# Kernel tuning notes

Measured on AMD Instinct MI355X. Metric: run time of the kernel, lower is better.

The kernel has to match this reference:

```python
import jax, jax.numpy as jnp
import numpy as np

N, M = 100000, 800000
F_IN, F_E, H = 64, 16, 64
T_NODE, T_EDGE = 2, 3
HEAD_DIM = 16.0


def setup_inputs() -> dict:
    key = jax.random.key(0)
    ks = jax.random.split(key, 16)
    inp = {
        "x": jax.random.normal(ks[0], (N, F_IN), jnp.float32),
        "edge_feat": jax.random.normal(ks[1], (M, F_E), jnp.float32),
        "node_type": jax.random.randint(ks[2], (N,), 0, T_NODE, jnp.int32),
        "edge_src": jax.random.randint(ks[3], (M,), 0, N, jnp.int32),
        "edge_dst": jax.random.randint(ks[4], (M,), 0, N, jnp.int32),
        "edge_type": jax.random.randint(ks[5], (M,), 0, T_EDGE, jnp.int32),
    }
    s_n = 1.0 / np.sqrt(F_IN)
    s_e = 1.0 / np.sqrt(F_E)
    for i, name in enumerate(["W1", "W2", "W3", "W4"]):
        inp[name] = jax.random.normal(ks[6 + i], (T_NODE, F_IN, H), jnp.float32) * s_n
        inp["b" + name[1]] = jax.random.normal(ks[10 + i], (T_NODE, H), jnp.float32) * 0.01
    inp["W5"] = jax.random.normal(ks[14], (T_EDGE, F_E, H), jnp.float32) * s_e
    inp["b5"] = jax.random.normal(ks[15], (T_EDGE, H), jnp.float32) * 0.01
    return inp


def _node_proj(x, W, b, node_type):
    # per-node-type linear: [T,F,H] weights, select row per node type
    p = jnp.einsum('nf,tfh->tnh', x, W) + b[:, None, :]      # [T,N,H]
    return jnp.take_along_axis(p, node_type[None, :, None], axis=0)[0]  # [N,H]


def reference(x, edge_feat, W1, b1, W2, b2, W3, b3, W4, b4, W5, b5,
              node_type, edge_src, edge_dst, edge_type):
    n = x.shape[0]
    h1 = _node_proj(x, W1, b1, node_type)
    h2 = _node_proj(x, W2, b2, node_type)
    h3 = _node_proj(x, W3, b3, node_type)
    h4 = _node_proj(x, W4, b4, node_type)
    # per-edge-type linear via weight gather (F_E is small)
    w5e = jnp.einsum('mf,mfh->mh', edge_feat, W5[edge_type]) + b5[edge_type]  # [M,H]
    # scalar attention logit per edge (w3_i . (w4_j + w5_ij)) / sqrt(head_dim)
    num = jnp.sum(h3[edge_dst] * (h4[edge_src] + w5e), axis=-1)  # [M]
    # softmax over a single scalar per edge == 1.0 exactly (faithful to source)
    score = jax.nn.softmax((num / jnp.sqrt(HEAD_DIM))[:, None], axis=-1)[:, 0]  # [M]
    msg = score[:, None] * (h2[edge_src] + w5e)                  # [M,H]
    out = h1 + jax.ops.segment_sum(msg, edge_dst, num_segments=n)
    return out
```

## Files before the change

kernel.cpp:

```cpp
#include <hip/hip_runtime.h>


#define CAP 16
#define OVF_CAP 32768

typedef __attribute__((ext_vector_type(8))) short short8;
typedef __attribute__((ext_vector_type(4))) float f32x4;

__device__ __forceinline__ float b2f(unsigned short u) {
    union { unsigned v; float f; } x; x.v = ((unsigned)u) << 16; return x.f;
}
__device__ __forceinline__ unsigned short f2b(float f) {
    union { float f; unsigned v; } x; x.f = f;
    unsigned u = x.v;
    unsigned r = (u + 0x7FFFu + ((u >> 16) & 1u)) >> 16;
    return (unsigned short)r;
}

__global__ __launch_bounds__(256) void k1_gemm_scatter(
    const float* __restrict__ x, const int* __restrict__ nt,
    const float* __restrict__ W1, const float* __restrict__ b1,
    const float* __restrict__ W2, const float* __restrict__ b2,
    const int* __restrict__ esrc, const int* __restrict__ edst,
    const int* __restrict__ etype,
    int* __restrict__ cnt32, int* __restrict__ ovfCnt,
    int4* __restrict__ ovf, int2* __restrict__ rec,
    float* __restrict__ out, unsigned short* __restrict__ h2b,
    int N, int M)
{
    __shared__ __align__(16) unsigned short sx[128 * 72];
    __shared__ __align__(16) unsigned short sw[4][64 * 72];
    __shared__ int snt[128];

    int tid = threadIdx.x;

    if (blockIdx.x & 1) {
        int e0 = (blockIdx.x >> 1) * 1024 + tid;
        int dd[4], ssrc[4], tty[4];
        bool v[4];
#pragma unroll
        for (int j = 0; j < 4; ++j) {
            int e = e0 + j * 256;
            v[j] = e < M;
            int ec = v[j] ? e : 0;
            dd[j]   = edst[ec];
            ssrc[j] = esrc[ec];
            tty[j]  = etype[ec];
        }
        int pos[4];
#pragma unroll
        for (int j = 0; j < 4; ++j)
            if (v[j]) pos[j] = atomicAdd(&cnt32[dd[j]], 1);
#pragma unroll
        for (int j = 0; j < 4; ++j) {
            if (!v[j]) continue;
            int packed = ssrc[j] | (tty[j] << 20);
            int e = e0 + j * 256;
            if (pos[j] < CAP) {
                rec[dd[j] * CAP + pos[j]] = make_int2(packed, e);
            } else {
                int slot = atomicAdd(ovfCnt, 1);
                if (slot < OVF_CAP) ovf[slot] = make_int4(packed, e, dd[j], 0);
            }
        }
        return;
    }

    int rowbase = (blockIdx.x >> 1) * 128;

    const float* Wm0 = W1;
    const float* Wm1 = W1 + 4096;
    const float* Wm2 = W2;
    const float* Wm3 = W2 + 4096;
#pragma unroll
    for (int j = 0; j < 4; ++j) {
        int k  = (tid >> 4) + j * 16;
        int n4 = (tid & 15) * 4;
        float4 w0 = *(const float4*)&Wm0[k * 64 + n4];
        float4 w1v = *(const float4*)&Wm1[k * 64 + n4];
        float4 w2v = *(const float4*)&Wm2[k * 64 + n4];
        float4 w3 = *(const float4*)&Wm3[k * 64 + n4];
        sw[0][(n4 + 0) * 72 + k] = f2b(w0.x);
        sw[0][(n4 + 1) * 72 + k] = f2b(w0.y);
        sw[0][(n4 + 2) * 72 + k] = f2b(w0.z);
        sw[0][(n4 + 3) * 72 + k] = f2b(w0.w);
        sw[1][(n4 + 0) * 72 + k] = f2b(w1v.x);
        sw[1][(n4 + 1) * 72 + k] = f2b(w1v.y);
        sw[1][(n4 + 2) * 72 + k] = f2b(w1v.z);
        sw[1][(n4 + 3) * 72 + k] = f2b(w1v.w);
        sw[2][(n4 + 0) * 72 + k] = f2b(w2v.x);
        sw[2][(n4 + 1) * 72 + k] = f2b(w2v.y);
        sw[2][(n4 + 2) * 72 + k] = f2b(w2v.z);
        sw[2][(n4 + 3) * 72 + k] = f2b(w2v.w);
        sw[3][(n4 + 0) * 72 + k] = f2b(w3.x);
        sw[3][(n4 + 1) * 72 + k] = f2b(w3.y);
        sw[3][(n4 + 2) * 72 + k] = f2b(w3.z);
        sw[3][(n4 + 3) * 72 + k] = f2b(w3.w);
    }

    if (tid < 128) {
        int r = rowbase + tid;
        snt[tid] = (r < N) ? nt[r] : 0;
    }

    int fr = (tid & 15) * 4;
    int ir = tid >> 4;
#pragma unroll
    for (int it = 0; it < 8; ++it) {
        int i = it * 16 + ir;
        int r = rowbase + i;
        float4 v = make_float4(0.f, 0.f, 0.f, 0.f);
        if (r < N) v = *(const float4*)&x[(size_t)r * 64 + fr];
        ushort4 p;
        p.x = f2b(v.x); p.y = f2b(v.y); p.z = f2b(v.z); p.w = f2b(v.w);
        *(ushort4*)&sx[i * 72 + fr] = p;
    }
    __syncthreads();

    int lane = tid & 63;
    int wid  = tid >> 6;
    int q    = lane >> 4;
    int cc   = lane & 15;
    int m0   = wid * 32;

    f32x4 acc[4][2][4];
#pragma unroll
    for (int mm = 0; mm < 4; ++mm)
#pragma unroll
        for (int s = 0; s < 2; ++s)
#pragma unroll
            for (int t = 0; t < 4; ++t)
                acc[mm][s][t] = (f32x4){0.f, 0.f, 0.f, 0.f};

#pragma unroll
    for (int k0 = 0; k0 < 64; k0 += 32) {
        int ko = k0 + q * 8;
        short8 af0 = *(short8*)&sx[(m0 + cc) * 72 + ko];
        short8 af1 = *(short8*)&sx[(m0 + 16 + cc) * 72 + ko];
#pragma unroll
        for (int mm = 0; mm < 4; ++mm)
#pragma unroll
            for (int t = 0; t < 4; ++t) {
                short8 bf = *(short8*)&sw[mm][(t * 16 + cc) * 72 + ko];
                acc[mm][0][t] = __builtin_amdgcn_mfma_f32_16x16x32_bf16(
                    af0, bf, acc[mm][0][t], 0, 0, 0);
                acc[mm][1][t] = __builtin_amdgcn_mfma_f32_16x16x32_bf16(
                    af1, bf, acc[mm][1][t], 0, 0, 0);
            }
    }

    float b1v[2][4], b2v[2][4];
#pragma unroll
    for (int ty = 0; ty < 2; ++ty)
#pragma unroll
        for (int t = 0; t < 4; ++t) {
            b1v[ty][t] = b1[ty * 64 + t * 16 + cc];
            b2v[ty][t] = b2[ty * 64 + t * 16 + cc];
        }

#pragma unroll
    for (int s = 0; s < 2; ++s)
#pragma unroll
        for (int reg = 0; reg < 4; ++reg) {
            int rl_ = m0 + s * 16 + q * 4 + reg;
            int r = rowbase + rl_;
            if (r < N) {
                int ty = snt[rl_];
#pragma unroll
                for (int t = 0; t < 4; ++t) {
                    float v1 = (ty ? acc[1][s][t][reg] : acc[0][s][t][reg])
                               + b1v[ty][t];
                    float v2 = (ty ? acc[3][s][t][reg] : acc[2][s][t][reg])
                               + b2v[ty][t];
                    out[(size_t)r * 64 + t * 16 + cc] = v1;
                    h2b[(size_t)r * 64 + t * 16 + cc] = f2b(v2);
                }
            }
        }
}

__global__ __launch_bounds__(256) void k2_gather_mm(
    const float* __restrict__ ef, const int2* __restrict__ rec,
    const int* __restrict__ cnt32,
    const float* __restrict__ W5, const float* __restrict__ b5,
    const int4* __restrict__ ovf, const int* __restrict__ ovfCnt,
    const unsigned short* __restrict__ h2b, float* __restrict__ out,
    int N, int gatherBlocks, int ovfBlocks)
{
    __shared__ __align__(16) unsigned short sa[32 * 136];
    __shared__ __align__(16) unsigned short swt[64 * 136];
    __shared__ __align__(16) float sH[32 * 66];

    int tid = threadIdx.x;
    int lane = tid & 63;
    int wid = tid >> 6;

    if (blockIdx.x >= (unsigned)gatherBlocks) {
        int novf = min(*ovfCnt, OVF_CAP);
        int gw = (blockIdx.x - gatherBlocks) * 4 + wid;
        int nw = ovfBlocks * 4;
        for (int ri = gw; ri < novf; ri += nw) {
            int4 o = ovf[ri];
            int s = o.x & 0xFFFFF;
            int t = (unsigned)o.x >> 20;
            float acc = b5[t * 64 + lane] + b2f(h2b[((size_t)s << 6) | lane]);
#pragma unroll
            for (int f = 0; f < 16; ++f)
                acc = fmaf(ef[(size_t)o.y * 16 + f],
                           W5[(t * 16 + f) * 64 + lane], acc);
            unsafeAtomicAdd(&out[(size_t)o.z * 64 + lane], acc);
        }
        return;
    }

#pragma unroll
    for (int k = 0; k < 13; ++k) {
        int idx = tid + k * 256;
        int j = idx >> 6;
        int h = idx & 63;
        float wv = 0.f;
        if (j < 48)      wv = W5[j * 64 + h];
        else if (j < 51) wv = b5[(j - 48) * 64 + h];
        unsigned short wb = f2b(wv);
        swt[h * 136 + j] = wb;
        swt[h * 136 + 52 + j] = wb;
    }
    {
        ushort4 z; z.x = 0; z.y = 0; z.z = 0; z.w = 0;
#pragma unroll
        for (int k = 0; k < 2; ++k) {
            int idx = tid + k * 256;
            if (idx < 384) {
                int h = idx / 6;
                int sp = (idx - h * 6) * 4;
                *(ushort4*)&swt[h * 136 + 104 + sp] = z;
            }
        }
        if (tid < 192) {
            int row = tid / 6;
            int sp = (tid - row * 6) * 4;
            *(ushort4*)&sa[row * 136 + 104 + sp] = z;
        }
    }

    int myt = (lane < 48) ? (lane >> 4) : (lane - 48);
    unsigned myf = lane & 15;
    bool fl = lane < 48;
    int wbase = blockIdx.x * 32 + wid * 8;

#pragma unroll 1
    for (int g = 0; g < 8; ++g) {
        int d = wbase + g;
        int dg = (d < N) ? min(cnt32[d], CAP) : 0;
        unsigned base = (unsigned)d * CAP;

        float accH = 0.f, accS = 0.f;
        float hLast = 0.f, vLast = 0.f;
        int tLast = -1;
        int dgm1 = dg - 1;

        for (int i = 0; i < dg; i += 8) {
            int2 r[8];
#pragma unroll
            for (int j = 0; j < 8; ++j) {
                int ij = min(i + j, dgm1);
                r[j] = rec[base + ij];
            }
            float hv[8], ev[8];
#pragma unroll
            for (int j = 0; j < 8; ++j) {
                unsigned s = (unsigned)r[j].x & 0xFFFFFu;
                hv[j] = b2f(h2b[((size_t)s << 6) | (unsigned)lane]);
                ev[j] = ef[((unsigned)r[j].y << 4) | myf];
            }
#pragma unroll
            for (int j = 0; j < 8; ++j) {
                int t = (int)((unsigned)r[j].x >> 20);
                float v = fl ? ev[j] : 1.0f;
                accH += hv[j];
                accS += (t == myt) ? v : 0.f;
                hLast = hv[j]; vLast = v; tLast = t;
            }
        }
        float fd = (float)(((dg + 7) & ~7) - dg);
        accH -= fd * hLast;
        accS -= (tLast == myt) ? fd * vLast : 0.f;

        int wd = wid * 8 + g;
        if (lane < 52) {
            unsigned short hi = f2b(accS);
            unsigned short lo = f2b(accS - b2f(hi));
            sa[wd * 136 + lane] = hi;
            sa[wd * 136 + 52 + lane] = lo;
        }
        sH[wd * 66 + lane] = accH;
    }
    __syncthreads();

    int q  = lane >> 4;
    int cc = lane & 15;
    int s  = wid & 1;
    int t0 = wid >> 1;

    f32x4 acc0 = (f32x4){0.f, 0.f, 0.f, 0.f};
    f32x4 acc1 = (f32x4){0.f, 0.f, 0.f, 0.f};
#pragma unroll
    for (int k0 = 0; k0 < 128; k0 += 32) {
        int ko = k0 + q * 8;
        short8 af = *(short8*)&sa[(s * 16 + cc) * 136 + ko];
        short8 bf0 = *(short8*)&swt[(t0 * 16 + cc) * 136 + ko];
        short8 bf1 = *(short8*)&swt[((t0 + 2) * 16 + cc) * 136 + ko];
        acc0 = __builtin_amdgcn_mfma_f32_16x16x32_bf16(af, bf0, acc0, 0, 0, 0);
        acc1 = __builtin_amdgcn_mfma_f32_16x16x32_bf16(af, bf1, acc1, 0, 0, 0);
    }

#pragma unroll
    for (int reg = 0; reg < 4; ++reg) {
        int rl = s * 16 + q * 4 + reg;
        int d = blockIdx.x * 32 + rl;
        if (d < N) {
            int c0 = t0 * 16 + cc;
            int c1 = (t0 + 2) * 16 + cc;
            float v0 = acc0[reg] + sH[rl * 66 + c0];
            float v1 = acc1[reg] + sH[rl * 66 + c1];
            unsafeAtomicAdd(&out[(size_t)d * 64 + c0], v0);
            unsafeAtomicAdd(&out[(size_t)d * 64 + c1], v1);
        }
    }
}

extern "C" void kernel_launch(void* const* d_in, const int* in_sizes, int n_in,
                              void* d_out, int out_size, void* d_ws, size_t ws_size,
                              hipStream_t stream) {
    const float* x  = (const float*)d_in[0];
    const float* ef = (const float*)d_in[1];
    const int* nt   = (const int*)d_in[2];
    const int* es   = (const int*)d_in[3];
    const int* ed   = (const int*)d_in[4];
    const int* et   = (const int*)d_in[5];
    const float* W1 = (const float*)d_in[6];
    const float* b1 = (const float*)d_in[7];
    const float* W2 = (const float*)d_in[8];
    const float* b2 = (const float*)d_in[9];
    const float* W5 = (const float*)d_in[14];
    const float* b5 = (const float*)d_in[15];

    int N = in_sizes[2];
    int M = in_sizes[3];

    char* w = (char*)d_ws;
    size_t off = 0;
    unsigned short* h2b = (unsigned short*)(w + off); off += (size_t)N * 64 * 2;
    off = (off + 255) & ~(size_t)255;
    int2* rec = (int2*)(w + off); off += (size_t)N * CAP * 8;
    off = (off + 255) & ~(size_t)255;
    int4* ovf = (int4*)(w + off); off += (size_t)OVF_CAP * 16;
    off = (off + 255) & ~(size_t)255;
    int* ovfCnt = (int*)(w + off);
    int* cnt32  = (int*)(w + off + 64);
    size_t zeroBytes = 64 + (size_t)N * 4;

    float* out = (float*)d_out;

    hipMemsetAsync(ovfCnt, 0, zeroBytes, stream);

    int gemmBlocks    = (N + 127) / 128;
    int scatterBlocks = (M + 1023) / 1024;
    int gb1 = 2 * max(gemmBlocks, scatterBlocks);
    k1_gemm_scatter<<<gb1, 256, 0, stream>>>(
        x, nt, W1, b1, W2, b2, es, ed, et,
        cnt32, ovfCnt, ovf, rec, out, h2b, N, M);

    int gatherBlocks = (N + 31) / 32;
    int ovfBlocks = 32;
    k2_gather_mm<<<gatherBlocks + ovfBlocks, 256, 0, stream>>>(
        ef, rec, cnt32, W5, b5, ovf, ovfCnt, h2b, out,
        N, gatherBlocks, ovfBlocks);
}
```

Measured before the change: 309.3 us.

## Batch two destination nodes per gather pass and skip atomics when no overflow

The gather loop now handles two destination nodes at a time. It issues all 16 record loads up front and then the h2 and edge-feature loads with per-slot masking, so more memory requests are in flight and the tail-correction arithmetic is gone. The duplicated weight tile in shared memory is replaced by a single 64-wide copy that both hi and lo halves of the split-bf16 A operand index into, which reduces LDS footprint and setup stores. Output accumulation uses plain read-modify-write instead of atomics when the node has no overflow edges, relying on the overflow blocks touching only nodes above CAP.

```diff
diff --git a/kernel.cpp b/kernel.cpp
--- a/kernel.cpp
+++ b/kernel.cpp
@@ -188,8 +188,9 @@
     int N, int gatherBlocks, int ovfBlocks)
 {
     __shared__ __align__(16) unsigned short sa[32 * 136];
-    __shared__ __align__(16) unsigned short swt[64 * 136];
+    __shared__ __align__(16) unsigned short swt[64 * 72];
     __shared__ __align__(16) float sH[32 * 66];
+    __shared__ int sCnt[32];
 
     int tid = threadIdx.x;
     int lane = tid & 63;
@@ -221,25 +222,20 @@
         float wv = 0.f;
         if (j < 48)      wv = W5[j * 64 + h];
         else if (j < 51) wv = b5[(j - 48) * 64 + h];
-        unsigned short wb = f2b(wv);
-        swt[h * 136 + j] = wb;
-        swt[h * 136 + 52 + j] = wb;
+        swt[h * 72 + j] = f2b(wv);
     }
     {
         ushort4 z; z.x = 0; z.y = 0; z.z = 0; z.w = 0;
-#pragma unroll
-        for (int k = 0; k < 2; ++k) {
-            int idx = tid + k * 256;
-            if (idx < 384) {
-                int h = idx / 6;
-                int sp = (idx - h * 6) * 4;
-                *(ushort4*)&swt[h * 136 + 104 + sp] = z;
-            }
+        if (tid < 192) {
+            int h = tid / 3;
+            int sp = (tid - h * 3) * 4;
+            *(ushort4*)&swt[h * 72 + 52 + sp] = z;
         }
         if (tid < 192) {
             int row = tid / 6;
-            int sp = (tid - row * 6) * 4;
-            *(ushort4*)&sa[row * 136 + 104 + sp] = z;
+            int w6 = tid - row * 6;
+            int sp = (w6 < 3) ? (52 + w6 * 4) : (116 + (w6 - 3) * 4);
+            *(ushort4*)&sa[row * 136 + sp] = z;
         }
     }
 
@@ -248,52 +244,110 @@
     bool fl = lane < 48;
     int wbase = blockIdx.x * 32 + wid * 8;
 
-#pragma unroll 1
+    int cnts[8];
+#pragma unroll
     for (int g = 0; g < 8; ++g) {
         int d = wbase + g;
-        int dg = (d < N) ? min(cnt32[d], CAP) : 0;
-        unsigned base = (unsigned)d * CAP;
-
-        float accH = 0.f, accS = 0.f;
-        float hLast = 0.f, vLast = 0.f;
-        int tLast = -1;
-        int dgm1 = dg - 1;
-
-        for (int i = 0; i < dg; i += 8) {
-            int2 r[8];
+        cnts[g] = (d < N) ? cnt32[d] : 0;
+    }
+    if (lane == 0) {
+#pragma unroll
+        for (int g = 0; g < 8; ++g) sCnt[wid * 8 + g] = cnts[g];
+    }
+
+#pragma unroll 1
+    for (int gp = 0; gp < 8; gp += 2) {
+        int dA = wbase + gp, dB = dA + 1;
+        int dgA = min(cnts[gp], CAP);
+        int dgB = min(cnts[gp + 1], CAP);
+        unsigned baseA = (unsigned)(dA < N ? dA : 0) * CAP;
+        unsigned baseB = (unsigned)(dB < N ? dB : 0) * CAP;
+
+        int2 rA[8], rB[8];
+#pragma unroll
+        for (int j = 0; j < 8; ++j) rA[j] = rec[baseA + j];
+#pragma unroll
+        for (int j = 0; j < 8; ++j) rB[j] = rec[baseB + j];
+
+        float hvA[8], evA[8], hvB[8], evB[8];
+#pragma unroll
+        for (int j = 0; j < 8; ++j) {
+            bool ok = j < dgA;
+            unsigned s = ok ? ((unsigned)rA[j].x & 0xFFFFFu) : 0u;
+            unsigned e = ok ? (unsigned)rA[j].y : 0u;
+            hvA[j] = b2f(h2b[((size_t)s << 6) | (unsigned)lane]);
+            evA[j] = ef[(e << 4) | myf];
+        }
+#pragma unroll
+        for (int j = 0; j < 8; ++j) {
+            bool ok = j < dgB;
+            unsigned s = ok ? ((unsigned)rB[j].x & 0xFFFFFu) : 0u;
+            unsigned e = ok ? (unsigned)rB[j].y : 0u;
+            hvB[j] = b2f(h2b[((size_t)s << 6) | (unsigned)lane]);
+            evB[j] = ef[(e << 4) | myf];
+        }
+
+        float accHA = 0.f, accSA = 0.f, accHB = 0.f, accSB = 0.f;
+#pragma unroll
+        for (int j = 0; j < 8; ++j) {
+            bool okA = j < dgA;
+            int tA = (int)((unsigned)rA[j].x >> 20);
+            accHA += okA ? hvA[j] : 0.f;
+            float vA = fl ? evA[j] : 1.0f;
+            accSA += (okA && tA == myt) ? vA : 0.f;
+            bool okB = j < dgB;
+            int tB = (int)((unsigned)rB[j].x >> 20);
+            accHB += okB ? hvB[j] : 0.f;
+            float vB = fl ? evB[j] : 1.0f;
+            accSB += (okB && tB == myt) ? vB : 0.f;
+        }
+
+        if (dgA > 8) {
+            int2 r2[8];
+#pragma unroll
+            for (int j = 0; j < 8; ++j)
+                r2[j] = rec[baseA + (unsigned)min(8 + j, dgA - 1)];
 #pragma unroll
             for (int j = 0; j < 8; ++j) {
-                int ij = min(i + j, dgm1);
-                r[j] = rec[base + ij];
-            }
-            float hv[8], ev[8];
+                unsigned s = (unsigned)r2[j].x & 0xFFFFFu;
+                float hv = b2f(h2b[((size_t)s << 6) | (unsigned)lane]);
+                float evv = ef[((unsigned)r2[j].y << 4) | myf];
+                int t = (int)((unsigned)r2[j].x >> 20);
+                bool ok = (8 + j) < dgA;
+                accHA += ok ? hv : 0.f;
+                float v = fl ? evv : 1.0f;
+                accSA += (ok && t == myt) ? v : 0.f;
+            }
+        }
+        if (dgB > 8) {
+            int2 r2[8];
+#pragma unroll
+            for (int j = 0; j < 8; ++j)
+                r2[j] = rec[baseB + (unsigned)min(8 + j, dgB - 1)];
 #pragma unroll
             for (int j = 0; j < 8; ++j) {
-                unsigned s = (unsigned)r[j].x & 0xFFFFFu;
-                hv[j] = b2f(h2b[((size_t)s << 6) | (unsigned)lane]);
-                ev[j] = ef[((unsigned)r[j].y << 4) | myf];
-            }
-#pragma unroll
-            for (int j = 0; j < 8; ++j) {
-                int t = (int)((unsigned)r[j].x >> 20);
-                float v = fl ? ev[j] : 1.0f;
-                accH += hv[j];
-                accS += (t == myt) ? v : 0.f;
-                hLast = hv[j]; vLast = v; tLast = t;
-            }
-        }
-        float fd = (float)(((dg + 7) & ~7) - dg);
-        accH -= fd * hLast;
-        accS -= (tLast == myt) ? fd * vLast : 0.f;
-
-        int wd = wid * 8 + g;
+                unsigned s = (unsigned)r2[j].x & 0xFFFFFu;
+                float hv = b2f(h2b[((size_t)s << 6) | (unsigned)lane]);
+                float evv = ef[((unsigned)r2[j].y << 4) | myf];
+                int t = (int)((unsigned)r2[j].x >> 20);
+                bool ok = (8 + j) < dgB;
+                accHB += ok ? hv : 0.f;
+                float v = fl ? evv : 1.0f;
+                accSB += (ok && t == myt) ? v : 0.f;
+            }
+        }
+
+        int wdA = wid * 8 + gp, wdB = wdA + 1;
         if (lane < 52) {
-            unsigned short hi = f2b(accS);
-            unsigned short lo = f2b(accS - b2f(hi));
-            sa[wd * 136 + lane] = hi;
-            sa[wd * 136 + 52 + lane] = lo;
-        }
-        sH[wd * 66 + lane] = accH;
+            unsigned short hiA = f2b(accSA);
+            sa[wdA * 136 + lane] = hiA;
+            sa[wdA * 136 + 64 + lane] = f2b(accSA - b2f(hiA));
+            unsigned short hiB = f2b(accSB);
+            sa[wdB * 136 + lane] = hiB;
+            sa[wdB * 136 + 64 + lane] = f2b(accSB - b2f(hiB));
+        }
+        sH[wdA * 66 + lane] = accHA;
+        sH[wdB * 66 + lane] = accHB;
     }
     __syncthreads();
 
@@ -307,9 +361,10 @@
 #pragma unroll
     for (int k0 = 0; k0 < 128; k0 += 32) {
         int ko = k0 + q * 8;
+        int kb = ko & 63;
         short8 af = *(short8*)&sa[(s * 16 + cc) * 136 + ko];
-        short8 bf0 = *(short8*)&swt[(t0 * 16 + cc) * 136 + ko];
-        short8 bf1 = *(short8*)&swt[((t0 + 2) * 16 + cc) * 136 + ko];
+        short8 bf0 = *(short8*)&swt[(t0 * 16 + cc) * 72 + kb];
+        short8 bf1 = *(short8*)&swt[((t0 + 2) * 16 + cc) * 72 + kb];
         acc0 = __builtin_amdgcn_mfma_f32_16x16x32_bf16(af, bf0, acc0, 0, 0, 0);
         acc1 = __builtin_amdgcn_mfma_f32_16x16x32_bf16(af, bf1, acc1, 0, 0, 0);
     }
@@ -323,8 +378,15 @@
             int c1 = (t0 + 2) * 16 + cc;
             float v0 = acc0[reg] + sH[rl * 66 + c0];
             float v1 = acc1[reg] + sH[rl * 66 + c1];
-            unsafeAtomicAdd(&out[(size_t)d * 64 + c0], v0);
-            unsafeAtomicAdd(&out[(size_t)d * 64 + c1], v1);
+            float* p0 = &out[(size_t)d * 64 + c0];
+            float* p1 = &out[(size_t)d * 64 + c1];
+            if (sCnt[rl] > CAP) {
+                unsafeAtomicAdd(p0, v0);
+                unsafeAtomicAdd(p1, v1);
+            } else {
+                *p0 += v0;
+                *p1 += v1;
+            }
         }
     }
 }
```

Measured after the change: 298.6 us. -3.5%, faster.
